# Performance work log

Measured on AMD Instinct MI355X. Metric: run time of the kernel, lower is better.

## Reference

```python
import jax, jax.numpy as jnp
import numpy as np

NUM_HEADS = 12
HIDDEN = 768
HEAD_DIM = HIDDEN // NUM_HEADS  # 64
B, S = 2, 2048


def setup_inputs() -> dict:
    key = jax.random.key(0)
    ks = jax.random.split(key, 8)
    inp = {
        "hidden_states": jax.random.normal(ks[0], (B, S, HIDDEN), dtype=jnp.float32),
        "attention_mask": jnp.zeros((B, 1, 1, S), dtype=jnp.float32),
        "Wq": jax.random.normal(ks[1], (HIDDEN, HIDDEN), dtype=jnp.float32) * 0.02,
        "bq": jnp.zeros((HIDDEN,), dtype=jnp.float32),
        "Wk": jax.random.normal(ks[2], (HIDDEN, HIDDEN), dtype=jnp.float32) * 0.02,
        "bk": jnp.zeros((HIDDEN,), dtype=jnp.float32),
        "Wv": jax.random.normal(ks[3], (HIDDEN, HIDDEN), dtype=jnp.float32) * 0.02,
        "bv": jnp.zeros((HIDDEN,), dtype=jnp.float32),
    }
    return inp


def _split_heads(x):
    # [B, S, H*d] -> [B, H, S, d]
    b, s, _ = x.shape
    return x.reshape(b, s, NUM_HEADS, HEAD_DIM).transpose(0, 2, 1, 3)


def reference(hidden_states, attention_mask, Wq, bq, Wk, bk, Wv, bv):
    # Q/K/V projections (nn.Linear: x @ W.T + b; W generated square so direct matmul is equivalent math)
    q = _split_heads(hidden_states @ Wq + bq)  # [B,H,S,d]
    k = _split_heads(hidden_states @ Wk + bk)
    v = _split_heads(hidden_states @ Wv + bv)

    scale = 1.0 / np.sqrt(HEAD_DIM).astype(np.float32)
    scores = jnp.einsum("bhqd,bhkd->bhqk", q, k) * scale  # [B,H,S,S]
    scores = scores + attention_mask  # additive mask, broadcast [B,1,1,S]
    probs = jax.nn.softmax(scores, axis=-1)
    # dropout prob = 0.0 -> identity (eval mode)
    ctx = jnp.einsum("bhqk,bhkd->bhqd", probs, v)  # [B,H,S,d]
    ctx = ctx.transpose(0, 2, 1, 3).reshape(hidden_states.shape[0], hidden_states.shape[1], HIDDEN)
    return ctx
```

## Files before the change

### kernel.cpp

```cpp
#include <hip/hip_runtime.h>

#define S_LEN 2048
#define HID   768
#define NH    12
#define HD    64
#define BATCH 2
#define GK    768
#define L2E   1.44269504088896340736f
#define QSCL  (0.125f * L2E)

typedef __attribute__((ext_vector_type(8))) short bf16x8;
typedef __attribute__((ext_vector_type(4))) float f32x4;
typedef __attribute__((ext_vector_type(4))) short s16x4;
typedef __attribute__((ext_vector_type(8))) short s16x8;

__device__ __forceinline__ unsigned short f2bf(float f) {
    union { float f; unsigned int u; } v; v.f = f;
    unsigned int r = v.u + 0x7fffu + ((v.u >> 16) & 1u);
    return (unsigned short)(r >> 16);
}
__device__ __forceinline__ unsigned short f2bf_hu(float f) {
    union { float f; unsigned int u; } v; v.f = f;
    return (unsigned short)((v.u + 0x8000u) >> 16);
}

#define GLL16(gp, lp) __builtin_amdgcn_global_load_lds( \
    (const __attribute__((address_space(1))) unsigned int*)(gp), \
    (__attribute__((address_space(3))) unsigned int*)(lp), 16, 0, 0)


__global__ __launch_bounds__(256) void prep_kernel(
    const float* __restrict__ X, const float* __restrict__ Wq,
    const float* __restrict__ Wk, const float* __restrict__ Wv,
    unsigned short* __restrict__ Xb, unsigned short* __restrict__ Wt) {
    __shared__ float T[32][33];
    int bid = blockIdx.x;
    if (bid < 3072) {
        int id = bid * 256 + threadIdx.x;
        float4 v = ((const float4*)X)[id];
        s16x4 o; o[0] = (short)f2bf(v.x); o[1] = (short)f2bf(v.y);
        o[2] = (short)f2bf(v.z); o[3] = (short)f2bf(v.w);
        ((s16x4*)Xb)[id] = o;
        return;
    }
    int t2 = bid - 3072;
    int mat = t2 / 576, t = t2 % 576;
    int tk = t / 24, tn = t % 24;
    const float* W = (mat == 0) ? Wq : (mat == 1) ? Wk : Wv;
    const float scl = (mat == 0) ? QSCL : 1.0f;
    int r  = threadIdx.x >> 3;
    int c4 = (threadIdx.x & 7) * 4;
    float4 v = *(const float4*)&W[(size_t)(tk*32 + r) * GK + tn*32 + c4];
    T[c4+0][r] = v.x; T[c4+1][r] = v.y; T[c4+2][r] = v.z; T[c4+3][r] = v.w;
    __syncthreads();
    s16x4 o;
    o[0] = (short)f2bf(T[r][c4+0] * scl); o[1] = (short)f2bf(T[r][c4+1] * scl);
    o[2] = (short)f2bf(T[r][c4+2] * scl); o[3] = (short)f2bf(T[r][c4+3] * scl);
    *(s16x4*)&Wt[(size_t)(mat*768 + tn*32 + r) * GK + tk*32 + c4] = o;
}

__global__ __launch_bounds__(256) void gemm_qkv(
    const unsigned short* __restrict__ Xb, const unsigned short* __restrict__ Wt,
    const float* __restrict__ bq, const float* __restrict__ bk,
    const float* __restrict__ bv,
    unsigned short* __restrict__ qb, unsigned short* __restrict__ kb,
    unsigned short* __restrict__ vb) {
    __shared__ __align__(16) unsigned short smem[12288];

    const int tid = threadIdx.x;
    const int bm = blockIdx.y * 128;
    const int bn = blockIdx.x * 64;
    const int w = tid >> 6, l = tid & 63, quad = l >> 4, lq = l & 15;
    const int wx = w & 1, wy = w >> 1;

    const int srow = l >> 3, schunk = ((l & 7) ^ (l >> 3)) * 8;
    const unsigned short* aga = Xb + (size_t)(bm + w*32 + srow) * GK + schunk;
    const unsigned short* bga = Wt + (size_t)(bn + w*16 + srow) * GK + schunk;

    const int c0 = ((quad)     ^ (lq & 7)) * 8;
    const int c1 = ((4 + quad) ^ (lq & 7)) * 8;

    f32x4 zero = {0.f, 0.f, 0.f, 0.f};
    f32x4 acc[4][2];
#pragma unroll
    for (int mi = 0; mi < 4; mi++)
#pragma unroll
        for (int ni = 0; ni < 2; ni++) acc[mi][ni] = zero;

    for (int k0 = 0; k0 < GK; k0 += 64) {
        __syncthreads();
#pragma unroll
        for (int i = 0; i < 4; i++)
            GLL16(aga + k0 + i*8*GK, &smem[(w*32 + i*8) * 64]);
#pragma unroll
        for (int i = 0; i < 2; i++)
            GLL16(bga + k0 + i*8*GK, &smem[8192 + (w*16 + i*8) * 64]);
        __syncthreads();
#pragma unroll
        for (int kh = 0; kh < 2; kh++) {
            const int cc = kh ? c1 : c0;
            bf16x8 a[4], b[2];
#pragma unroll
            for (int mi = 0; mi < 4; mi++)
                a[mi] = *(const bf16x8*)&smem[(wy*64 + mi*16 + lq) * 64 + cc];
#pragma unroll
            for (int ni = 0; ni < 2; ni++)
                b[ni] = *(const bf16x8*)&smem[8192 + (wx*32 + ni*16 + lq) * 64 + cc];
#pragma unroll
            for (int mi = 0; mi < 4; mi++)
#pragma unroll
                for (int ni = 0; ni < 2; ni++)
                    acc[mi][ni] = __builtin_amdgcn_mfma_f32_16x16x32_bf16(
                        a[mi], b[ni], acc[mi][ni], 0, 0, 0);
        }
    }
    __syncthreads();

    const int mat = bn / 768;
    const float* bias = (mat == 0) ? bq : (mat == 1) ? bk : bv;
    const float bscl = (mat == 0) ? QSCL : 1.0f;
    const int nbase = bn % 768;
    const int h  = nbase >> 6;
    const int b_ = bm >> 11, s0 = bm & 2047;

    if (mat != 1) {
#pragma unroll
        for (int ni = 0; ni < 2; ni++) {
            int nl = wx*32 + ni*16 + lq;
            float bval = bias[nbase + nl] * bscl;
#pragma unroll
            for (int mi = 0; mi < 4; mi++) {
                int m0 = wy*64 + mi*16 + quad*4;
                s16x4 pk;
#pragma unroll
                for (int r = 0; r < 4; r++) pk[r] = (short)f2bf_hu(acc[mi][ni][r] + bval);
                *(s16x4*)&smem[nl*136 + m0] = pk;
            }
        }
        __syncthreads();
        unsigned short* outp = (mat == 0) ? qb : vb;
        unsigned short* obase = outp + ((size_t)((b_*NH + h) * HD)) * S_LEN + s0;
#pragma unroll
        for (int i = 0; i < 4; i++) {
            int id = i * 256 + tid;
            int n = id >> 4, c = id & 15;
            *(s16x8*)&obase[(size_t)n * S_LEN + c*8] = *(const s16x8*)&smem[n*136 + c*8];
        }
    } else {
#pragma unroll
        for (int ni = 0; ni < 2; ni++) {
            int nl = wx*32 + ni*16 + lq;
            float bval = bias[nbase + nl];
#pragma unroll
            for (int mi = 0; mi < 4; mi++) {
                int m0 = wy*64 + mi*16 + quad*4;
#pragma unroll
                for (int r = 0; r < 4; r++)
                    smem[(m0 + r)*66 + nl] = f2bf_hu(acc[mi][ni][r] + bval);
            }
        }
        __syncthreads();
        unsigned short* obase = kb + ((size_t)((b_*NH + h) * S_LEN + s0)) * HD;
#pragma unroll
        for (int i = 0; i < 4; i++) {
            int id = i * 256 + tid;
            int m = id >> 3, c = id & 7;
            *(s16x8*)&obase[(size_t)m * HD + c*8] = *(const s16x8*)&smem[m*66 + c*8];
        }
    }
}

__global__ __launch_bounds__(256) void attn_kernel(
    const unsigned short* __restrict__ Qtg, const unsigned short* __restrict__ Kg,
    const unsigned short* __restrict__ Vtg, const float* __restrict__ maskg,
    float* __restrict__ out) {
    __shared__ __align__(16) unsigned short Ks[2][64][64];
    __shared__ __align__(16) unsigned short Vt[2][64][64];
    __shared__ __align__(16) unsigned short Ps[4][16][72];
    __shared__ __align__(16) float mkL[S_LEN];

    const int tid = threadIdx.x;
    const int w = tid >> 6, l = tid & 63, quad = l >> 4, lq = l & 15;
    const int bh = blockIdx.y;
    const int q0 = blockIdx.x * 64;
    const int bi = bh / NH, hi = bh % NH;
    const unsigned short* Kh = Kg + (size_t)bh * S_LEN * HD;
    const unsigned short* Vh = Vtg + (size_t)bh * HD * S_LEN;

    bf16x8 a0, a1;
    {
        const unsigned short* Qt = Qtg + (size_t)bh * HD * S_LEN + (q0 + w*16 + lq);
#pragma unroll
        for (int j = 0; j < 8; j++) {
            a0[j] = (short)Qt[(size_t)(quad*8 + j) * S_LEN];
            a1[j] = (short)Qt[(size_t)(quad*8 + j + 32) * S_LEN];
        }
    }

    {
        const float4* mb4 = (const float4*)(maskg + (size_t)bi * S_LEN);
#pragma unroll
        for (int i = 0; i < 2; i++) {
            int idx = i * 256 + tid;
            float4 v = mb4[idx];
            float4 sv; sv.x = v.x*L2E; sv.y = v.y*L2E; sv.z = v.z*L2E; sv.w = v.w*L2E;
            ((float4*)mkL)[idx] = sv;
        }
    }

    bf16x8 ones;
#pragma unroll
    for (int i = 0; i < 8; i++) ones[i] = (short)0x3F80;

    const int srow = l >> 3, schunk = ((l & 7) ^ (l >> 3)) * 8;
    const unsigned short* kga = Kh + (size_t)(w*16 + srow) * HD + schunk;
    const unsigned short* vga = Vh + (size_t)(w*16 + srow) * S_LEN + schunk;

    const int c0 = ((quad)     ^ (lq & 7)) * 8;
    const int c1 = ((4 + quad) ^ (lq & 7)) * 8;

    f32x4 zero = {0.f, 0.f, 0.f, 0.f};
    f32x4 o[4], lsum = zero;
#pragma unroll
    for (int ng = 0; ng < 4; ng++) o[ng] = zero;

    auto stage = [&](int buf, int kt) {
#pragma unroll
        for (int i = 0; i < 2; i++) {
            GLL16(kga + (size_t)kt*64*HD + i*8*HD, &Ks[buf][w*16 + i*8][0]);
            GLL16(vga + kt*64 + (size_t)i*8*S_LEN, &Vt[buf][w*16 + i*8][0]);
        }
    };

    auto compute = [&](int buf, int kt) {
        const int kk = kt * 64;
        float mm[4];
#pragma unroll
        for (int g = 0; g < 4; g++) mm[g] = mkL[kk + g*16 + lq];

        f32x4 s[4];
#pragma unroll
        for (int g = 0; g < 4; g++) {
            bf16x8 b0 = *(const bf16x8*)&Ks[buf][g*16 + lq][c0];
            bf16x8 b1 = *(const bf16x8*)&Ks[buf][g*16 + lq][c1];
            f32x4 z = __builtin_amdgcn_mfma_f32_16x16x32_bf16(a0, b0, zero, 0, 0, 0);
            s[g]    = __builtin_amdgcn_mfma_f32_16x16x32_bf16(a1, b1, z,    0, 0, 0);
        }

#pragma unroll
        for (int g = 0; g < 4; g++) {
            const int col = g*16 + lq;
#pragma unroll
            for (int r = 0; r < 4; r++)
                Ps[w][quad*4 + r][col] = f2bf_hu(exp2f(s[g][r] + mm[g]));
        }

        bf16x8 pa0 = *(const bf16x8*)&Ps[w][lq][quad*8];
        bf16x8 pa1 = *(const bf16x8*)&Ps[w][lq][32 + quad*8];

        lsum = __builtin_amdgcn_mfma_f32_16x16x32_bf16(pa0, ones, lsum, 0, 0, 0);
        lsum = __builtin_amdgcn_mfma_f32_16x16x32_bf16(pa1, ones, lsum, 0, 0, 0);

#pragma unroll
        for (int ng = 0; ng < 4; ng++) {
            bf16x8 v0 = *(const bf16x8*)&Vt[buf][ng*16 + lq][c0];
            bf16x8 v1 = *(const bf16x8*)&Vt[buf][ng*16 + lq][c1];
            f32x4 t = __builtin_amdgcn_mfma_f32_16x16x32_bf16(pa0, v0, o[ng], 0, 0, 0);
            o[ng]   = __builtin_amdgcn_mfma_f32_16x16x32_bf16(pa1, v1, t,     0, 0, 0);
        }
    };

    stage(0, 0);
    __syncthreads();

    for (int kt = 0; kt < S_LEN / 64; kt += 2) {
        stage(1, kt + 1);
        compute(0, kt);
        __syncthreads();
        if (kt + 2 < S_LEN / 64) stage(0, kt + 2);
        compute(1, kt + 1);
        __syncthreads();
    }

#pragma unroll
    for (int r = 0; r < 4; r++) {
        const float inv = 1.0f / lsum[r];
        const int row = q0 + w*16 + quad*4 + r;
#pragma unroll
        for (int ng = 0; ng < 4; ng++)
            out[((size_t)(bi * S_LEN + row)) * HID + hi*HD + ng*16 + lq] = o[ng][r] * inv;
    }
}

extern "C" void kernel_launch(void* const* d_in, const int* in_sizes, int n_in,
                              void* d_out, int out_size, void* d_ws, size_t ws_size,
                              hipStream_t stream) {
    const float* X    = (const float*)d_in[0];
    const float* mask = (const float*)d_in[1];
    const float* Wq   = (const float*)d_in[2];
    const float* bq   = (const float*)d_in[3];
    const float* Wk   = (const float*)d_in[4];
    const float* bk   = (const float*)d_in[5];
    const float* Wv   = (const float*)d_in[6];
    const float* bv   = (const float*)d_in[7];
    float* out = (float*)d_out;

    const size_t per = (size_t)BATCH * NH * S_LEN * HD;
    unsigned short* qb = (unsigned short*)d_ws;
    unsigned short* kb = qb + per;
    unsigned short* vb = kb + per;
    unsigned short* xb = vb + per;
    unsigned short* wt = xb + (size_t)4096 * GK;

    prep_kernel<<<4800, 256, 0, stream>>>(X, Wq, Wk, Wv, xb, wt);

    dim3 ggrid(2304 / 64, 4096 / 128);
    gemm_qkv<<<ggrid, 256, 0, stream>>>(xb, wt, bq, bk, bv, qb, kb, vb);

    dim3 agrid(S_LEN / 64, BATCH * NH);
    attn_kernel<<<agrid, 256, 0, stream>>>(qb, kb, vb, mask, out);
}
```

Baseline: 163.0 us.

## Double-buffer shared-memory tiles in QKV projection GEMM K-loop

The QKV GEMM now keeps two shared-memory buffers for A and B tiles. It issues the global-to-LDS load for the next K-slice before running the MFMA work on the current slice, and uses one barrier per slice instead of two. The aim is to hide global load latency behind matrix math. In exchange, the kernel's LDS footprint doubles, which may reduce occupancy, and the epilogue now reuses the A buffer as staging space.

```diff
diff --git a/kernel.cpp b/kernel.cpp
--- a/kernel.cpp
+++ b/kernel.cpp
@@ -65,7 +65,8 @@
     const float* __restrict__ bv,
     unsigned short* __restrict__ qb, unsigned short* __restrict__ kb,
     unsigned short* __restrict__ vb) {
-    __shared__ __align__(16) unsigned short smem[12288];
+    __shared__ __align__(16) unsigned short As[2][128][64];
+    __shared__ __align__(16) unsigned short Bs[2][64][64];
 
     const int tid = threadIdx.x;
     const int bm = blockIdx.y * 128;
@@ -87,25 +88,27 @@
 #pragma unroll
         for (int ni = 0; ni < 2; ni++) acc[mi][ni] = zero;
 
-    for (int k0 = 0; k0 < GK; k0 += 64) {
-        __syncthreads();
+    auto stage = [&](int buf, int ks) {
+        const int k0 = ks * 64;
 #pragma unroll
         for (int i = 0; i < 4; i++)
-            GLL16(aga + k0 + i*8*GK, &smem[(w*32 + i*8) * 64]);
+            GLL16(aga + k0 + i*8*GK, &As[buf][w*32 + i*8][0]);
 #pragma unroll
         for (int i = 0; i < 2; i++)
-            GLL16(bga + k0 + i*8*GK, &smem[8192 + (w*16 + i*8) * 64]);
-        __syncthreads();
+            GLL16(bga + k0 + i*8*GK, &Bs[buf][w*16 + i*8][0]);
+    };
+
+    auto compute = [&](int buf) {
 #pragma unroll
         for (int kh = 0; kh < 2; kh++) {
             const int cc = kh ? c1 : c0;
             bf16x8 a[4], b[2];
 #pragma unroll
             for (int mi = 0; mi < 4; mi++)
-                a[mi] = *(const bf16x8*)&smem[(wy*64 + mi*16 + lq) * 64 + cc];
+                a[mi] = *(const bf16x8*)&As[buf][wy*64 + mi*16 + lq][cc];
 #pragma unroll
             for (int ni = 0; ni < 2; ni++)
-                b[ni] = *(const bf16x8*)&smem[8192 + (wx*32 + ni*16 + lq) * 64 + cc];
+                b[ni] = *(const bf16x8*)&Bs[buf][wx*32 + ni*16 + lq][cc];
 #pragma unroll
             for (int mi = 0; mi < 4; mi++)
 #pragma unroll
@@ -113,9 +116,20 @@
                     acc[mi][ni] = __builtin_amdgcn_mfma_f32_16x16x32_bf16(
                         a[mi], b[ni], acc[mi][ni], 0, 0, 0);
         }
-    }
+    };
+
+    stage(0, 0);
     __syncthreads();
-
+    for (int ks = 0; ks < GK / 64; ks += 2) {
+        stage(1, ks + 1);
+        compute(0);
+        __syncthreads();
+        if (ks + 2 < GK / 64) stage(0, ks + 2);
+        compute(1);
+        __syncthreads();
+    }
+
+    unsigned short* ep = (unsigned short*)As;
     const int mat = bn / 768;
     const float* bias = (mat == 0) ? bq : (mat == 1) ? bk : bv;
     const float bscl = (mat == 0) ? QSCL : 1.0f;
@@ -134,7 +148,7 @@
                 s16x4 pk;
 #pragma unroll
                 for (int r = 0; r < 4; r++) pk[r] = (short)f2bf_hu(acc[mi][ni][r] + bval);
-                *(s16x4*)&smem[nl*136 + m0] = pk;
+                *(s16x4*)&ep[nl*136 + m0] = pk;
             }
         }
         __syncthreads();
@@ -144,7 +158,7 @@
         for (int i = 0; i < 4; i++) {
             int id = i * 256 + tid;
             int n = id >> 4, c = id & 15;
-            *(s16x8*)&obase[(size_t)n * S_LEN + c*8] = *(const s16x8*)&smem[n*136 + c*8];
+            *(s16x8*)&obase[(size_t)n * S_LEN + c*8] = *(const s16x8*)&ep[n*136 + c*8];
         }
     } else {
 #pragma unroll
@@ -156,7 +170,7 @@
                 int m0 = wy*64 + mi*16 + quad*4;
 #pragma unroll
                 for (int r = 0; r < 4; r++)
-                    smem[(m0 + r)*66 + nl] = f2bf_hu(acc[mi][ni][r] + bval);
+                    ep[(m0 + r)*66 + nl] = f2bf_hu(acc[mi][ni][r] + bval);
             }
         }
         __syncthreads();
@@ -165,7 +179,7 @@
         for (int i = 0; i < 4; i++) {
             int id = i * 256 + tid;
             int m = id >> 3, c = id & 7;
-            *(s16x8*)&obase[(size_t)m * HD + c*8] = *(const s16x8*)&smem[m*66 + c*8];
+            *(s16x8*)&obase[(size_t)m * HD + c*8] = *(const s16x8*)&ep[m*66 + c*8];
         }
     }
 }
```

Result: no change. 162.3 us (-0.4%).
